# Kernel optimization log

Hardware: AMD Instinct MI355X
Metric: run time of the kernel (lower is better)

## Reference

```python
import jax, jax.numpy as jnp
import numpy as np

B, N, H, W = 128, 16384, 512, 512  # frames, points/frame, image height/width


def setup_inputs() -> dict:
    key = jax.random.key(0)
    k1, k2 = jax.random.split(key)
    pts = jax.random.uniform(k1, (B, N, 3), dtype=jnp.float32)
    # columns: x in [0, W-1], y in [0, H-1], intensity in [0, 1]
    outputs = jnp.concatenate(
        [pts[..., 0:1] * (W - 1), pts[..., 1:2] * (H - 1), pts[..., 2:3]], axis=-1
    )
    targets = jax.random.uniform(k2, (B, H, W), dtype=jnp.float32)
    return {"outputs": outputs, "targets": targets}


def _rasterize(outputs, h, w):
    """Bilinear splat of (x, y, intensity) points into a [B, h, w] image."""
    b, n, _ = outputs.shape
    x = jnp.clip(outputs[..., 0], 0.0, w - 1)
    y = jnp.clip(outputs[..., 1], 0.0, h - 1)
    inten = outputs[..., 2]
    x0f = jnp.floor(x)
    y0f = jnp.floor(y)
    fx = x - x0f  # fractional offsets -> bilinear weights
    fy = y - y0f
    x0 = x0f.astype(jnp.int32)
    y0 = y0f.astype(jnp.int32)
    x1 = jnp.minimum(x0 + 1, w - 1)
    y1 = jnp.minimum(y0 + 1, h - 1)
    bidx = jnp.broadcast_to(jnp.arange(b, dtype=jnp.int32)[:, None], (b, n))
    img = jnp.zeros((b, h, w), dtype=outputs.dtype)
    img = img.at[bidx, y0, x0].add(inten * (1 - fx) * (1 - fy))
    img = img.at[bidx, y0, x1].add(inten * fx * (1 - fy))
    img = img.at[bidx, y1, x0].add(inten * (1 - fx) * fy)
    img = img.at[bidx, y1, x1].add(inten * fx * fy)
    return img


def reference(outputs, targets):
    h, w = targets.shape[1], targets.shape[2]
    output_image = _rasterize(outputs, h, w)
    return jnp.mean((output_image - targets) ** 2)
```

## Files before the change

### kernel.cpp

```cpp
#include <hip/hip_runtime.h>

constexpr int B = 128;
constexpr int N = 16384;
constexpr int H = 512;
constexpr int W = 512;
constexpr int HW = H * W;
constexpr long long TOT = (long long)B * HW;

constexpr int TROWS = 16;
constexpr int NTILES = H / TROWS;
constexpr int NBUCKETS = B * NTILES;
constexpr int CAP = 1024;
constexpr int NGROUPS = B * N / 4;
constexpr int BIN_BLOCKS = NGROUPS / 512;
constexpr int TILE_F4 = TROWS * W / 4;
constexpr int F4_PER_THREAD = TILE_F4 / 512;

__device__ __forceinline__ void lds_add(float* p, float v) {
    __hip_atomic_fetch_add(p, v, __ATOMIC_RELAXED, __HIP_MEMORY_SCOPE_WORKGROUP);
}

__global__ void __launch_bounds__(512) k_bin(const float4* __restrict__ pts,
                                             float4* __restrict__ buckets,
                                             unsigned int* __restrict__ cnt) {
    __shared__ unsigned int lcnt[NTILES];
    __shared__ unsigned int lbase[NTILES];

    int tid = blockIdx.x * 512 + threadIdx.x;
    int frame = tid >> 12;
    int fb = frame * NTILES;

    if (threadIdx.x < NTILES) lcnt[threadIdx.x] = 0;
    __syncthreads();

    float4 a = pts[tid * 3 + 0];
    float4 b = pts[tid * 3 + 1];
    float4 c = pts[tid * 3 + 2];

    float xs[4] = {a.x, a.w, b.z, c.y};
    float ys[4] = {a.y, b.x, b.w, c.z};
    float is[4] = {a.z, b.y, c.x, c.w};

    int tb0[4], sl0[4], tb1[4], sl1[4];
#pragma unroll
    for (int k = 0; k < 4; ++k) {
        float x = fminf(fmaxf(xs[k], 0.0f), (float)(W - 1));
        float y = fminf(fmaxf(ys[k], 0.0f), (float)(H - 1));
        xs[k] = x; ys[k] = y;
        int y0 = (int)floorf(y);
        int y1 = min(y0 + 1, H - 1);
        int t0 = y0 >> 4;
        int t1 = y1 >> 4;
        tb0[k] = t0;
        sl0[k] = (int)atomicAdd(&lcnt[t0], 1u);
        if (t1 != t0) {
            tb1[k] = t1;
            sl1[k] = (int)atomicAdd(&lcnt[t1], 1u);
        } else {
            tb1[k] = -1; sl1[k] = 0;
        }
    }
    __syncthreads();

    if (threadIdx.x < NTILES)
        lbase[threadIdx.x] = atomicAdd(&cnt[fb + threadIdx.x], lcnt[threadIdx.x]);
    __syncthreads();

#pragma unroll
    for (int k = 0; k < 4; ++k) {
        float4 rec = make_float4(xs[k], ys[k], is[k], 0.0f);
        unsigned s0 = lbase[tb0[k]] + (unsigned)sl0[k];
        if (s0 < (unsigned)CAP)
            buckets[(size_t)(fb + tb0[k]) * CAP + s0] = rec;
        if (tb1[k] >= 0) {
            unsigned s1 = lbase[tb1[k]] + (unsigned)sl1[k];
            if (s1 < (unsigned)CAP)
                buckets[(size_t)(fb + tb1[k]) * CAP + s1] = rec;
        }
    }
}

__global__ void __launch_bounds__(512) k_tile(const float4* __restrict__ buckets,
                                              const unsigned int* __restrict__ cnt,
                                              const float* __restrict__ tgt,
                                              double* __restrict__ partials) {
    __shared__ float tile[TROWS * W];
    __shared__ double sacc[8];
    int bid = blockIdx.x;
    int frame = bid >> 5;
    int t = bid & (NTILES - 1);
    int r0 = t * TROWS;

    float4* t4 = (float4*)tile;
#pragma unroll
    for (int k = 0; k < F4_PER_THREAD; ++k)
        t4[threadIdx.x + k * 512] = make_float4(0.f, 0.f, 0.f, 0.f);

    int n = (int)min(cnt[bid], (unsigned)CAP);
    __syncthreads();

    const float4* tg = (const float4*)(tgt + (size_t)frame * HW + (size_t)r0 * W);
    float4 tv0 = tg[threadIdx.x];
    float4 tv1 = tg[threadIdx.x + 512];
    float4 tv2 = tg[threadIdx.x + 1024];
    float4 tv3 = tg[threadIdx.x + 1536];

    const float4* bp = buckets + (size_t)bid * CAP;
    for (int i = threadIdx.x; i < n; i += 512) {
        float4 p = bp[i];
        float x = p.x, y = p.y, inten = p.z;
        float x0f = floorf(x), y0f = floorf(y);
        float fx = x - x0f, fy = y - y0f;
        int x0 = (int)x0f, y0 = (int)y0f;
        int x1 = min(x0 + 1, W - 1);
        int y1 = min(y0 + 1, H - 1);
        int ra = y0 - r0;
        int rb = y1 - r0;
        float w00 = inten * (1.0f - fx) * (1.0f - fy);
        float w01 = inten * fx * (1.0f - fy);
        float w10 = inten * (1.0f - fx) * fy;
        float w11 = inten * fx * fy;
        if ((unsigned)ra < (unsigned)TROWS) {
            lds_add(&tile[ra * W + x0], w00);
            lds_add(&tile[ra * W + x1], w01);
        }
        if ((unsigned)rb < (unsigned)TROWS) {
            lds_add(&tile[rb * W + x0], w10);
            lds_add(&tile[rb * W + x1], w11);
        }
    }
    __syncthreads();

    double acc = 0.0;
    {
        float4 sv = t4[threadIdx.x];
        float d0 = sv.x - tv0.x, d1 = sv.y - tv0.y, d2 = sv.z - tv0.z, d3 = sv.w - tv0.w;
        acc += (double)(d0 * d0 + d1 * d1) + (double)(d2 * d2 + d3 * d3);
        sv = t4[threadIdx.x + 512];
        d0 = sv.x - tv1.x; d1 = sv.y - tv1.y; d2 = sv.z - tv1.z; d3 = sv.w - tv1.w;
        acc += (double)(d0 * d0 + d1 * d1) + (double)(d2 * d2 + d3 * d3);
        sv = t4[threadIdx.x + 1024];
        d0 = sv.x - tv2.x; d1 = sv.y - tv2.y; d2 = sv.z - tv2.z; d3 = sv.w - tv2.w;
        acc += (double)(d0 * d0 + d1 * d1) + (double)(d2 * d2 + d3 * d3);
        sv = t4[threadIdx.x + 1536];
        d0 = sv.x - tv3.x; d1 = sv.y - tv3.y; d2 = sv.z - tv3.z; d3 = sv.w - tv3.w;
        acc += (double)(d0 * d0 + d1 * d1) + (double)(d2 * d2 + d3 * d3);
    }

    for (int off = 32; off > 0; off >>= 1)
        acc += __shfl_down(acc, off, 64);
    int lane = threadIdx.x & 63;
    int wave = threadIdx.x >> 6;
    if (lane == 0) sacc[wave] = acc;
    __syncthreads();
    if (threadIdx.x == 0) {
        double s = 0.0;
#pragma unroll
        for (int wv = 0; wv < 8; ++wv) s += sacc[wv];
        partials[bid] = s;
    }
}

__global__ void __launch_bounds__(256) k_final(const double* __restrict__ partials,
                                               float* __restrict__ out) {
    double acc = 0.0;
    for (int i = threadIdx.x; i < NBUCKETS; i += 256)
        acc += partials[i];
    for (int off = 32; off > 0; off >>= 1)
        acc += __shfl_down(acc, off, 64);
    __shared__ double sacc[4];
    int lane = threadIdx.x & 63;
    int wave = threadIdx.x >> 6;
    if (lane == 0) sacc[wave] = acc;
    __syncthreads();
    if (threadIdx.x == 0) {
        double s = sacc[0] + sacc[1] + sacc[2] + sacc[3];
        out[0] = (float)(s / (double)TOT);
    }
}

extern "C" void kernel_launch(void* const* d_in, const int* in_sizes, int n_in,
                              void* d_out, int out_size, void* d_ws, size_t ws_size,
                              hipStream_t stream) {
    const float* pts = (const float*)d_in[0];
    const float* tgt = (const float*)d_in[1];
    float* out = (float*)d_out;

    unsigned int* cnt = (unsigned int*)d_ws;
    double* partials = (double*)((char*)d_ws + 16384);
    float4* buckets = (float4*)((char*)d_ws + 65536);

    hipMemsetAsync(cnt, 0, NBUCKETS * sizeof(unsigned int), stream);
    k_bin<<<BIN_BLOCKS, 512, 0, stream>>>((const float4*)pts, buckets, cnt);
    k_tile<<<NBUCKETS, 512, 0, stream>>>(buckets, cnt, tgt, partials);
    k_final<<<1, 256, 0, stream>>>(partials, out);
}
```

Before: 86.35 us.

## Replace global bucket counters with fixed per-block segments padded with zeros

Binning now writes each block's points into a private fixed-size segment (128 slots per tile per bin block) and pads unused slots with zero-intensity records. This removes the global atomic counters, the memset and the count read. The tile kernel then processes exactly 1024 records per tile with no loop bounds. The cost is extra zero-fill writes and splat work on padding records. Points are silently dropped if a block's segment for one tile overflows its 128 slots.

```diff
diff --git a/kernel.cpp b/kernel.cpp
--- a/kernel.cpp
+++ b/kernel.cpp
@@ -10,78 +10,87 @@
 constexpr int TROWS = 16;
 constexpr int NTILES = H / TROWS;
 constexpr int NBUCKETS = B * NTILES;
-constexpr int CAP = 1024;
-constexpr int NGROUPS = B * N / 4;
-constexpr int BIN_BLOCKS = NGROUPS / 512;
-constexpr int TILE_F4 = TROWS * W / 4;
-constexpr int F4_PER_THREAD = TILE_F4 / 512;
+constexpr int BLK_PER_FRAME = 8;
+constexpr int BIN_BLOCKS = B * BLK_PER_FRAME;
+constexpr int KSEG = 128;
+
+__global__ void __launch_bounds__(512) k_bin(const float4* __restrict__ pts,
+                                             float4* __restrict__ buckets) {
+    __shared__ unsigned int lcnt[NTILES];
+    int bid = blockIdx.x;
+    int frame = bid >> 3;
+    int blk = bid & 7;
+    int g = bid * 512 + threadIdx.x;
+
+    if (threadIdx.x < NTILES) lcnt[threadIdx.x] = 0;
+    __syncthreads();
+
+    float4 a = pts[g * 3 + 0];
+    float4 b = pts[g * 3 + 1];
+    float4 c = pts[g * 3 + 2];
+
+    float xs[4] = {a.x, a.w, b.z, c.y};
+    float ys[4] = {a.y, b.x, b.w, c.z};
+    float is[4] = {a.z, b.y, c.x, c.w};
+
+    size_t fbase = ((size_t)frame * NTILES * BLK_PER_FRAME + blk) * KSEG;
+#pragma unroll
+    for (int k = 0; k < 4; ++k) {
+        float x = fminf(fmaxf(xs[k], 0.0f), (float)(W - 1));
+        float y = fminf(fmaxf(ys[k], 0.0f), (float)(H - 1));
+        int y0 = (int)floorf(y);
+        int y1 = min(y0 + 1, H - 1);
+        int t0 = y0 >> 4;
+        int t1 = y1 >> 4;
+        float4 rec = make_float4(x, y, is[k], 0.0f);
+        unsigned s0 = atomicAdd(&lcnt[t0], 1u);
+        if (s0 < (unsigned)KSEG)
+            buckets[fbase + (size_t)t0 * (BLK_PER_FRAME * KSEG) + s0] = rec;
+        if (t1 != t0) {
+            unsigned s1 = atomicAdd(&lcnt[t1], 1u);
+            if (s1 < (unsigned)KSEG)
+                buckets[fbase + (size_t)t1 * (BLK_PER_FRAME * KSEG) + s1] = rec;
+        }
+    }
+    __syncthreads();
+
+    int team = threadIdx.x >> 4;
+    int lane = threadIdx.x & 15;
+    unsigned start = min(lcnt[team], (unsigned)KSEG);
+    float4* seg = buckets + fbase + (size_t)team * (BLK_PER_FRAME * KSEG);
+    float4 z = make_float4(0.f, 0.f, 0.f, 0.f);
+    for (int s = (int)start + lane; s < KSEG; s += 16)
+        seg[s] = z;
+}
 
 __device__ __forceinline__ void lds_add(float* p, float v) {
     __hip_atomic_fetch_add(p, v, __ATOMIC_RELAXED, __HIP_MEMORY_SCOPE_WORKGROUP);
 }
 
-__global__ void __launch_bounds__(512) k_bin(const float4* __restrict__ pts,
-                                             float4* __restrict__ buckets,
-                                             unsigned int* __restrict__ cnt) {
-    __shared__ unsigned int lcnt[NTILES];
-    __shared__ unsigned int lbase[NTILES];
-
-    int tid = blockIdx.x * 512 + threadIdx.x;
-    int frame = tid >> 12;
-    int fb = frame * NTILES;
-
-    if (threadIdx.x < NTILES) lcnt[threadIdx.x] = 0;
-    __syncthreads();
-
-    float4 a = pts[tid * 3 + 0];
-    float4 b = pts[tid * 3 + 1];
-    float4 c = pts[tid * 3 + 2];
-
-    float xs[4] = {a.x, a.w, b.z, c.y};
-    float ys[4] = {a.y, b.x, b.w, c.z};
-    float is[4] = {a.z, b.y, c.x, c.w};
-
-    int tb0[4], sl0[4], tb1[4], sl1[4];
-#pragma unroll
-    for (int k = 0; k < 4; ++k) {
-        float x = fminf(fmaxf(xs[k], 0.0f), (float)(W - 1));
-        float y = fminf(fmaxf(ys[k], 0.0f), (float)(H - 1));
-        xs[k] = x; ys[k] = y;
-        int y0 = (int)floorf(y);
-        int y1 = min(y0 + 1, H - 1);
-        int t0 = y0 >> 4;
-        int t1 = y1 >> 4;
-        tb0[k] = t0;
-        sl0[k] = (int)atomicAdd(&lcnt[t0], 1u);
-        if (t1 != t0) {
-            tb1[k] = t1;
-            sl1[k] = (int)atomicAdd(&lcnt[t1], 1u);
-        } else {
-            tb1[k] = -1; sl1[k] = 0;
-        }
+__device__ __forceinline__ void splat(float4 p, float* __restrict__ tile, int r0) {
+    float x = p.x, y = p.y, inten = p.z;
+    float x0f = floorf(x), y0f = floorf(y);
+    float fx = x - x0f, fy = y - y0f;
+    int x0 = (int)x0f, y0 = (int)y0f;
+    int x1 = min(x0 + 1, W - 1);
+    int y1 = min(y0 + 1, H - 1);
+    int ra = y0 - r0;
+    int rb = y1 - r0;
+    float w00 = inten * (1.0f - fx) * (1.0f - fy);
+    float w01 = inten * fx * (1.0f - fy);
+    float w10 = inten * (1.0f - fx) * fy;
+    float w11 = inten * fx * fy;
+    if ((unsigned)ra < (unsigned)TROWS) {
+        lds_add(&tile[ra * W + x0], w00);
+        lds_add(&tile[ra * W + x1], w01);
     }
-    __syncthreads();
-
-    if (threadIdx.x < NTILES)
-        lbase[threadIdx.x] = atomicAdd(&cnt[fb + threadIdx.x], lcnt[threadIdx.x]);
-    __syncthreads();
-
-#pragma unroll
-    for (int k = 0; k < 4; ++k) {
-        float4 rec = make_float4(xs[k], ys[k], is[k], 0.0f);
-        unsigned s0 = lbase[tb0[k]] + (unsigned)sl0[k];
-        if (s0 < (unsigned)CAP)
-            buckets[(size_t)(fb + tb0[k]) * CAP + s0] = rec;
-        if (tb1[k] >= 0) {
-            unsigned s1 = lbase[tb1[k]] + (unsigned)sl1[k];
-            if (s1 < (unsigned)CAP)
-                buckets[(size_t)(fb + tb1[k]) * CAP + s1] = rec;
-        }
+    if ((unsigned)rb < (unsigned)TROWS) {
+        lds_add(&tile[rb * W + x0], w10);
+        lds_add(&tile[rb * W + x1], w11);
     }
 }
 
 __global__ void __launch_bounds__(512) k_tile(const float4* __restrict__ buckets,
-                                              const unsigned int* __restrict__ cnt,
                                               const float* __restrict__ tgt,
                                               double* __restrict__ partials) {
     __shared__ float tile[TROWS * W];
@@ -91,44 +100,24 @@
     int t = bid & (NTILES - 1);
     int r0 = t * TROWS;
 
-    float4* t4 = (float4*)tile;
-#pragma unroll
-    for (int k = 0; k < F4_PER_THREAD; ++k)
-        t4[threadIdx.x + k * 512] = make_float4(0.f, 0.f, 0.f, 0.f);
-
-    int n = (int)min(cnt[bid], (unsigned)CAP);
-    __syncthreads();
-
+    const float4* bp = buckets + (size_t)bid * (BLK_PER_FRAME * KSEG);
+    float4 p0 = bp[threadIdx.x];
+    float4 p1 = bp[threadIdx.x + 512];
     const float4* tg = (const float4*)(tgt + (size_t)frame * HW + (size_t)r0 * W);
     float4 tv0 = tg[threadIdx.x];
     float4 tv1 = tg[threadIdx.x + 512];
     float4 tv2 = tg[threadIdx.x + 1024];
     float4 tv3 = tg[threadIdx.x + 1536];
 
-    const float4* bp = buckets + (size_t)bid * CAP;
-    for (int i = threadIdx.x; i < n; i += 512) {
-        float4 p = bp[i];
-        float x = p.x, y = p.y, inten = p.z;
-        float x0f = floorf(x), y0f = floorf(y);
-        float fx = x - x0f, fy = y - y0f;
-        int x0 = (int)x0f, y0 = (int)y0f;
-        int x1 = min(x0 + 1, W - 1);
-        int y1 = min(y0 + 1, H - 1);
-        int ra = y0 - r0;
-        int rb = y1 - r0;
-        float w00 = inten * (1.0f - fx) * (1.0f - fy);
-        float w01 = inten * fx * (1.0f - fy);
-        float w10 = inten * (1.0f - fx) * fy;
-        float w11 = inten * fx * fy;
-        if ((unsigned)ra < (unsigned)TROWS) {
-            lds_add(&tile[ra * W + x0], w00);
-            lds_add(&tile[ra * W + x1], w01);
-        }
-        if ((unsigned)rb < (unsigned)TROWS) {
-            lds_add(&tile[rb * W + x0], w10);
-            lds_add(&tile[rb * W + x1], w11);
-        }
-    }
+    float4* t4 = (float4*)tile;
+    float4 z = make_float4(0.f, 0.f, 0.f, 0.f);
+#pragma unroll
+    for (int k = 0; k < 4; ++k)
+        t4[threadIdx.x + k * 512] = z;
+    __syncthreads();
+
+    splat(p0, tile, r0);
+    splat(p1, tile, r0);
     __syncthreads();
 
     double acc = 0.0;
@@ -161,20 +150,22 @@
     }
 }
 
-__global__ void __launch_bounds__(256) k_final(const double* __restrict__ partials,
+__global__ void __launch_bounds__(512) k_final(const double* __restrict__ partials,
                                                float* __restrict__ out) {
     double acc = 0.0;
-    for (int i = threadIdx.x; i < NBUCKETS; i += 256)
+    for (int i = threadIdx.x; i < NBUCKETS; i += 512)
         acc += partials[i];
     for (int off = 32; off > 0; off >>= 1)
         acc += __shfl_down(acc, off, 64);
-    __shared__ double sacc[4];
+    __shared__ double sacc[8];
     int lane = threadIdx.x & 63;
     int wave = threadIdx.x >> 6;
     if (lane == 0) sacc[wave] = acc;
     __syncthreads();
     if (threadIdx.x == 0) {
-        double s = sacc[0] + sacc[1] + sacc[2] + sacc[3];
+        double s = 0.0;
+#pragma unroll
+        for (int wv = 0; wv < 8; ++wv) s += sacc[wv];
         out[0] = (float)(s / (double)TOT);
     }
 }
@@ -186,12 +177,10 @@
     const float* tgt = (const float*)d_in[1];
     float* out = (float*)d_out;
 
-    unsigned int* cnt = (unsigned int*)d_ws;
-    double* partials = (double*)((char*)d_ws + 16384);
+    double* partials = (double*)d_ws;
     float4* buckets = (float4*)((char*)d_ws + 65536);
 
-    hipMemsetAsync(cnt, 0, NBUCKETS * sizeof(unsigned int), stream);
-    k_bin<<<BIN_BLOCKS, 512, 0, stream>>>((const float4*)pts, buckets, cnt);
-    k_tile<<<NBUCKETS, 512, 0, stream>>>(buckets, cnt, tgt, partials);
-    k_final<<<1, 256, 0, stream>>>(partials, out);
+    k_bin<<<BIN_BLOCKS, 512, 0, stream>>>((const float4*)pts, buckets);
+    k_tile<<<NBUCKETS, 512, 0, stream>>>(buckets, tgt, partials);
+    k_final<<<1, 512, 0, stream>>>(partials, out);
 }
```

Measured after the change: 128.0 us. +48.2%, slower.
